# Kernel optimization log

Hardware: AMD Instinct MI355X
Metric: run time of the kernel (lower is better)

The kernel has to match this reference:

```python
import jax, jax.numpy as jnp
import numpy as np

H = 1200  # hidden size
I = 30    # input feature size


def _gru_layer(x_seq, h0, W_ih, W_hh, b_ih, b_hh):
    """x_seq: [T, B, I_in]; h0: [B, H]. PyTorch gate order (r, z, n)."""
    def step(h, x_t):
        gi = x_t @ W_ih.T + b_ih          # [B, 3H]
        gh = h @ W_hh.T + b_hh            # [B, 3H]
        i_r, i_z, i_n = jnp.split(gi, 3, axis=-1)
        h_r, h_z, h_n = jnp.split(gh, 3, axis=-1)
        r = jax.nn.sigmoid(i_r + h_r)
        z = jax.nn.sigmoid(i_z + h_z)
        n = jnp.tanh(i_n + r * h_n)
        h_new = (1.0 - z) * n + z * h
        return h_new, h_new
    h_last, outs = jax.lax.scan(step, h0, x_seq)
    return outs, h_last  # outs: [T, B, H]


def setup_inputs() -> dict:
    key = jax.random.key(0)
    ks = jax.random.split(key, 9)
    k = 1.0 / np.sqrt(H)
    u = lambda kk, shape: jax.random.uniform(kk, shape, jnp.float32, -k, k)
    x = jax.random.normal(ks[0], (64, 512, I), dtype=jnp.float32)
    return {
        "x": x,
        "W_ih0": u(ks[1], (3 * H, I)),
        "W_hh0": u(ks[2], (3 * H, H)),
        "b_ih0": u(ks[3], (3 * H,)),
        "b_hh0": u(ks[4], (3 * H,)),
        "W_ih1": u(ks[5], (3 * H, H)),
        "W_hh1": u(ks[6], (3 * H, H)),
        "b_ih1": u(ks[7], (3 * H,)),
        "b_hh1": u(ks[8], (3 * H,)),
    }


def reference(x, W_ih0, W_hh0, b_ih0, b_hh0, W_ih1, W_hh1, b_ih1, b_hh1):
    B = x.shape[0]
    x_tb = jnp.transpose(x, (1, 0, 2))  # [T, B, I]
    h0 = jnp.zeros((B, H), dtype=x.dtype)
    out0, h_last0 = _gru_layer(x_tb, h0, W_ih0, W_hh0, b_ih0, b_hh0)
    out1, h_last1 = _gru_layer(out0, h0, W_ih1, W_hh1, b_ih1, b_hh1)
    h_n = jnp.stack([h_last0, h_last1], axis=0)  # [2, B, H]
    return h_n
```

## Files before the change

kernel.cpp:

```cpp
#include <hip/hip_runtime.h>
#include <hip/hip_bf16.h>


#define Hh 1200
#define HP 1280
#define TT 512
#define II 30
#define KS_TOT 38
#define KS_PW 5
#define NTG 75
#define NBLK 225
#define NTHR 512

typedef __attribute__((ext_vector_type(8))) short short8;
typedef __attribute__((ext_vector_type(4))) float f32x4;

#define SZ_WF 17510400ull
#define OFF_WHH0 0ull
#define OFF_WIH1 SZ_WF
#define OFF_WHH1 (2ull*SZ_WF)
#define OFF_STATE (3ull*SZ_WF)
#define SZ_HF 307200ull
#define SZ_HB 163840ull
#define SZ_GX 921600ull
#define OFF_H0F OFF_STATE
#define OFF_H1F (OFF_H0F + SZ_HF)
#define OFF_H0B (OFF_H1F + SZ_HF)
#define OFF_H1B (OFF_H0B + 2ull*SZ_HB)
#define OFF_GX  (OFF_H1B + 2ull*SZ_HB)
#define STATE_BYTES (2ull*SZ_HF + 4ull*SZ_HB + 2ull*SZ_GX)
#define OFF_BAR (OFF_STATE + STATE_BYTES)
#define WS_NEEDED (OFF_BAR + 16384ull)

__device__ __forceinline__ unsigned short f2bf(float f){
  unsigned u = __float_as_uint(f);
  unsigned r = u + 0x7FFFu + ((u >> 16) & 1u);
  return (unsigned short)(r >> 16);
}
__device__ __forceinline__ float bf2f(unsigned short s){
  return __uint_as_float(((unsigned)s) << 16);
}
__device__ __forceinline__ float sigmoid_f(float v){ return 1.f/(1.f + __expf(-v)); }
__device__ __forceinline__ float tanh_f(float v){ float e = __expf(2.f*v); return 1.f - 2.f/(e + 1.f); }
__device__ __forceinline__ unsigned long long pack2f(float a, float b){
  union { float f[2]; unsigned long long u; } v; v.f[0]=a; v.f[1]=b; return v.u;
}
__device__ __forceinline__ short8 aload16(const unsigned short* p){
  union { unsigned long long u[2]; short8 s; } v;
  const unsigned long long* q = (const unsigned long long*)p;
  v.u[0] = __hip_atomic_load(q,     __ATOMIC_RELAXED, __HIP_MEMORY_SCOPE_AGENT);
  v.u[1] = __hip_atomic_load(q + 1, __ATOMIC_RELAXED, __HIP_MEMORY_SCOPE_AGENT);
  return v.s;
}
__device__ __forceinline__ void aload2f(const float* p, float* f0, float* f1){
  union { unsigned long long u; float f[2]; } v;
  v.u = __hip_atomic_load((const unsigned long long*)p, __ATOMIC_RELAXED, __HIP_MEMORY_SCOPE_AGENT);
  *f0 = v.f[0]; *f1 = v.f[1];
}

__global__ void prep_w(const float* __restrict__ W, unsigned short* __restrict__ Wf){
  int blk = blockIdx.x;
  int nt = blk / KS_TOT, ks = blk - nt*KS_TOT;
  int l = threadIdx.x;
  int n = nt*16 + (l & 15);
  int k0 = ks*32 + (l >> 4)*8;
  alignas(16) unsigned short hi[8];
  alignas(16) unsigned short lo[8];
  #pragma unroll
  for (int j = 0; j < 8; j++){
    int k = k0 + j;
    float w = (k < Hh) ? W[(size_t)n*Hh + k] : 0.f;
    unsigned short h16 = f2bf(w);
    hi[j] = h16;
    lo[j] = f2bf(w - bf2f(h16));
  }
  size_t cbase = ((size_t)(nt*KS_TOT + ks))*1024ull;
  *(short8*)(Wf + cbase + (size_t)l*8)        = *(const short8*)hi;
  *(short8*)(Wf + cbase + 512 + (size_t)l*8)  = *(const short8*)lo;
}

__global__ void init_state(char* __restrict__ ws){
  size_t i = (size_t)blockIdx.x*256 + threadIdx.x;
  size_t n_all = (STATE_BYTES + 16384ull)/16ull;
  if (i < n_all){
    f32x4 z = {0.f,0.f,0.f,0.f};
    ((f32x4*)(ws + OFF_STATE))[i] = z;
  }
}

__global__ void __launch_bounds__(NTHR)
__attribute__((amdgpu_waves_per_eu(2)))
gru_persist(
    char* __restrict__ ws,
    const float* __restrict__ x,
    const float* __restrict__ Wih0,
    const float* __restrict__ bih0, const float* __restrict__ bhh0,
    const float* __restrict__ bih1, const float* __restrict__ bhh1)
{
  const int bid  = blockIdx.x;
  const int role = bid / NTG;
  const int nb   = bid - role*NTG;
  const int tid  = threadIdx.x;
  const int wv   = tid >> 6;
  const int lane = tid & 63;
  const int col  = lane & 15;
  const int kg   = lane >> 4;
  const int ks0  = wv * KS_PW;
  const int eb  = tid >> 3;
  const int ecp = tid & 7;
  const int c0  = ecp*2;
  const int gc0 = nb*16 + c0;
  const int lastS = (role == 0) ? (TT-1) : (TT+1);

  __shared__ float part[12][8][256];
  __shared__ float red[12][256];
  __shared__ float xl[64][II];
  __shared__ float wl[48][II];
  __shared__ float hfl[64][16];

  int* bar_flags = (int*)(ws + OFF_BAR);

  for (int i = tid; i < 64*16; i += NTHR) ((float*)hfl)[i] = 0.f;

  const short8* wt = (const short8*)(ws + ((role==0)?OFF_WHH0:(role==1)?OFF_WIH1:OFF_WHH1));
  short8 wfr[3][KS_PW][2];
  #pragma unroll
  for (int g = 0; g < 3; g++)
    #pragma unroll
    for (int k = 0; k < KS_PW; k++){
      int ks = ks0 + k;
      #pragma unroll
      for (int sp = 0; sp < 2; sp++){
        short8 v = {0,0,0,0,0,0,0,0};
        if (ks < KS_TOT)
          v = wt[((size_t)((g*NTG + nb)*KS_TOT + ks))*128 + sp*64 + lane];
        wfr[g][k][sp] = v;
        asm("" : "+v"(wfr[g][k][sp]));
      }
    }

  if (role == 0){
    for (int i = tid; i < 48*II; i += NTHR){
      int rl = i/II, c = i - rl*II;
      int g = rl >> 4, cl = rl & 15;
      wl[rl][c] = Wih0[(size_t)(g*Hh + nb*16 + cl)*II + c];
    }
  }

  float bIv[3][2] = {{0.f,0.f},{0.f,0.f},{0.f,0.f}};
  float bHv[3][2] = {{0.f,0.f},{0.f,0.f},{0.f,0.f}};
  if (role == 0){
    #pragma unroll
    for (int g = 0; g < 3; g++){
      bIv[g][0] = bih0[g*Hh + gc0]; bIv[g][1] = bih0[g*Hh + gc0 + 1];
      bHv[g][0] = bhh0[g*Hh + gc0]; bHv[g][1] = bhh0[g*Hh + gc0 + 1];
    }
  } else if (role == 1){
    #pragma unroll
    for (int g = 0; g < 3; g++){
      bIv[g][0] = bih1[g*Hh + gc0]; bIv[g][1] = bih1[g*Hh + gc0 + 1];
    }
  } else {
    #pragma unroll
    for (int g = 0; g < 3; g++){
      bHv[g][0] = bhh1[g*Hh + gc0]; bHv[g][1] = bhh1[g*Hh + gc0 + 1];
    }
  }

  for (int s = 0; s < TT + 2; s++){
    const bool active = (role==0) ? (s < TT) : (role==1) ? (s >= 1 && s <= TT) : (s >= 2);
    const int t   = s - role;
    const int par = t & 1;

    if (active){
      const unsigned short* Ab;
      if (role == 0)      Ab = (const unsigned short*)(ws + OFF_H0B + (size_t)par*SZ_HB);
      else if (role == 1) Ab = (const unsigned short*)(ws + OFF_H0B + (size_t)((t+1)&1)*SZ_HB);
      else                Ab = (const unsigned short*)(ws + OFF_H1B + (size_t)par*SZ_HB);

      if (role == 0){
        for (int i = tid; i < 64*II; i += NTHR){
          int b = i/II, c = i - b*II;
          xl[b][c] = x[(size_t)b*(TT*II) + t*II + c];
        }
      }

      f32x4 acc[3][4];
      #pragma unroll
      for (int g = 0; g < 3; g++)
        #pragma unroll
        for (int m = 0; m < 4; m++) acc[g][m] = (f32x4){0.f,0.f,0.f,0.f};

      #pragma unroll
      for (int k = 0; k < KS_PW; k++){
        short8 a[4];
        #pragma unroll
        for (int m = 0; m < 4; m++)
          a[m] = aload16(&Ab[(size_t)(m*16 + col)*HP + (ks0 + k)*32 + kg*8]);
        #pragma unroll
        for (int g = 0; g < 3; g++)
          #pragma unroll
          for (int m = 0; m < 4; m++){
            acc[g][m] = __builtin_amdgcn_mfma_f32_16x16x32_bf16(a[m], wfr[g][k][0], acc[g][m], 0,0,0);
            acc[g][m] = __builtin_amdgcn_mfma_f32_16x16x32_bf16(a[m], wfr[g][k][1], acc[g][m], 0,0,0);
          }
      }
      #pragma unroll
      for (int g = 0; g < 3; g++)
        #pragma unroll
        for (int m = 0; m < 4; m++)
          *(f32x4*)&part[g*4 + m][wv][lane*4] = acc[g][m];
    }
    __syncthreads();

    if (active){
      #pragma unroll
      for (int r = 0; r < 6; r++){
        int o = r*NTHR + tid;
        int tile = o >> 8, e = o & 255;
        float v = part[tile][0][e] + part[tile][1][e] + part[tile][2][e] + part[tile][3][e]
                + part[tile][4][e] + part[tile][5][e] + part[tile][6][e] + part[tile][7][e];
        red[tile][e] = v;
      }
    }
    __syncthreads();

    if (active){
      const int mt = eb >> 4, dr = eb & 15;
      const int e0 = ((dr>>2)<<6) | (c0<<2) | (dr&3);
      if (role == 1){
        float* gxo = (float*)(ws + OFF_GX + (size_t)par*SZ_GX);
        #pragma unroll
        for (int g = 0; g < 3; g++){
          float v0 = red[g*4+mt][e0]     + bIv[g][0];
          float v1 = red[g*4+mt][e0 + 4] + bIv[g][1];
          __hip_atomic_store((unsigned long long*)&gxo[(size_t)eb*3600 + g*Hh + gc0],
                             pack2f(v0, v1), __ATOMIC_RELAXED, __HIP_MEMORY_SCOPE_AGENT);
        }
      } else {
        float gxv[3][2];
        if (role == 0){
          #pragma unroll
          for (int g = 0; g < 3; g++)
            #pragma unroll
            for (int j = 0; j < 2; j++){
              float sum = bIv[g][j];
              #pragma unroll
              for (int i = 0; i < II; i++) sum += wl[g*16 + c0 + j][i] * xl[eb][i];
              gxv[g][j] = sum;
            }
        } else {
          const float* gxi = (const float*)(ws + OFF_GX + (size_t)par*SZ_GX);
          #pragma unroll
          for (int g = 0; g < 3; g++)
            aload2f(&gxi[(size_t)eb*3600 + g*Hh + gc0], &gxv[g][0], &gxv[g][1]);
        }
        unsigned short* hbout = (unsigned short*)(ws + ((role==0)?OFF_H0B:OFF_H1B)
                                                   + (size_t)(par^1)*SZ_HB);
        float hq[2];
        unsigned short hb[2];
        #pragma unroll
        for (int j = 0; j < 2; j++){
          int e = e0 + j*4;
          float rr = sigmoid_f(red[mt][e]     + gxv[0][j] + bHv[0][j]);
          float zz = sigmoid_f(red[4+mt][e]   + gxv[1][j] + bHv[1][j]);
          float nn = tanh_f(gxv[2][j] + rr*(red[8+mt][e] + bHv[2][j]));
          float hold = hfl[eb][c0 + j];
          float hn = (1.f - zz)*nn + zz*hold;
          hfl[eb][c0 + j] = hn;
          hq[j] = hn;
          hb[j] = f2bf(hn);
        }
        unsigned pk = (unsigned)hb[0] | ((unsigned)hb[1] << 16);
        __hip_atomic_store((unsigned*)&hbout[(size_t)eb*HP + gc0], pk,
                           __ATOMIC_RELAXED, __HIP_MEMORY_SCOPE_AGENT);
        if (s == lastS){
          float* hfin = (float*)(ws + ((role==0)?OFF_H0F:OFF_H1F));
          hfin[(size_t)eb*Hh + gc0]     = hq[0];
          hfin[(size_t)eb*Hh + gc0 + 1] = hq[1];
        }
      }
    }

    __syncthreads();
    if (tid == 0){
      asm volatile("s_waitcnt vmcnt(0)" ::: "memory");
      __hip_atomic_store(&bar_flags[bid*16], s+1, __ATOMIC_RELAXED, __HIP_MEMORY_SCOPE_AGENT);
    }
    if (tid < NBLK){
      while (__hip_atomic_load(&bar_flags[tid*16], __ATOMIC_RELAXED, __HIP_MEMORY_SCOPE_AGENT) < s+1)
        __builtin_amdgcn_s_sleep(1);
    }
    asm volatile("" ::: "memory");
    __syncthreads();
  }
}

__global__ void write_out(const char* __restrict__ ws, float* __restrict__ out){
  int i = blockIdx.x*256 + threadIdx.x;
  if (i < 76800)        out[i] = *(const float*)(ws + OFF_H0F + (size_t)i*4);
  else if (i < 153600)  out[i] = *(const float*)(ws + OFF_H1F + (size_t)(i - 76800)*4);
}

extern "C" void kernel_launch(void* const* d_in, const int* in_sizes, int n_in,
                              void* d_out, int out_size, void* d_ws, size_t ws_size,
                              hipStream_t stream)
{
  const float* x    = (const float*)d_in[0];
  const float* Wih0 = (const float*)d_in[1];
  const float* Whh0 = (const float*)d_in[2];
  const float* bih0 = (const float*)d_in[3];
  const float* bhh0 = (const float*)d_in[4];
  const float* Wih1 = (const float*)d_in[5];
  const float* Whh1 = (const float*)d_in[6];
  const float* bih1 = (const float*)d_in[7];
  const float* bhh1 = (const float*)d_in[8];
  char* ws = (char*)d_ws;
  if (ws_size < WS_NEEDED) return;

  dim3 pgrid(NBLK*KS_TOT);
  prep_w<<<pgrid, 64, 0, stream>>>(Whh0, (unsigned short*)(ws + OFF_WHH0));
  prep_w<<<pgrid, 64, 0, stream>>>(Wih1, (unsigned short*)(ws + OFF_WIH1));
  prep_w<<<pgrid, 64, 0, stream>>>(Whh1, (unsigned short*)(ws + OFF_WHH1));
  init_state<<<764, 256, 0, stream>>>(ws);

  gru_persist<<<NBLK, NTHR, 0, stream>>>(ws, x, Wih0, bih0, bhh0, bih1, bhh1);

  write_out<<<600, 256, 0, stream>>>(ws, (float*)d_out);
}
```

Baseline: 7.442 ms.

## Replace global all-block barrier with per-role dependency flags and deeper buffers

Drops the 225-block global barrier run every step. Each role group (layer0 recurrent, layer1 input projection, layer1 recurrent) now waits only on the flags of the producers it depends on, with acquire/release fences, and the hidden-state buffers go from 2 to 4 so producers can run ahead of consumers. The final hidden states are written straight to the output, so the separate write_out kernel and the fp32 state buffers are removed. This cuts barrier wait and lets the layers pipeline more loosely, but the multi-buffer flag protocol is harder to get right and can race or deadlock if any wait bound is off.

```diff
diff --git a/kernel.cpp b/kernel.cpp
--- a/kernel.cpp
+++ b/kernel.cpp
@@ -19,18 +19,13 @@
 #define OFF_WHH0 0ull
 #define OFF_WIH1 SZ_WF
 #define OFF_WHH1 (2ull*SZ_WF)
-#define OFF_STATE (3ull*SZ_WF)
-#define SZ_HF 307200ull
 #define SZ_HB 163840ull
 #define SZ_GX 921600ull
-#define OFF_H0F OFF_STATE
-#define OFF_H1F (OFF_H0F + SZ_HF)
-#define OFF_H0B (OFF_H1F + SZ_HF)
-#define OFF_H1B (OFF_H0B + 2ull*SZ_HB)
-#define OFF_GX  (OFF_H1B + 2ull*SZ_HB)
-#define STATE_BYTES (2ull*SZ_HF + 4ull*SZ_HB + 2ull*SZ_GX)
-#define OFF_BAR (OFF_STATE + STATE_BYTES)
-#define WS_NEEDED (OFF_BAR + 16384ull)
+#define OFF_H0B (3ull*SZ_WF)
+#define OFF_H1B (OFF_H0B + 4ull*SZ_HB)
+#define OFF_GX  (OFF_H1B + 4ull*SZ_HB)
+#define OFF_BAR (OFF_GX + 2ull*SZ_GX)
+#define WS_NEEDED (OFF_BAR + 4096ull)
 
 __device__ __forceinline__ unsigned short f2bf(float f){
   unsigned u = __float_as_uint(f);
@@ -57,6 +52,11 @@
   v.u = __hip_atomic_load((const unsigned long long*)p, __ATOMIC_RELAXED, __HIP_MEMORY_SCOPE_AGENT);
   *f0 = v.f[0]; *f1 = v.f[1];
 }
+
+#define POLLGE(addr, thr) \
+  while (__hip_atomic_load((addr), __ATOMIC_RELAXED, __HIP_MEMORY_SCOPE_AGENT) < (thr)) \
+    __builtin_amdgcn_s_sleep(1)
+#define ACQ() __builtin_amdgcn_fence(__ATOMIC_ACQUIRE, "agent")
 
 __global__ void prep_w(const float* __restrict__ W, unsigned short* __restrict__ Wf){
   int blk = blockIdx.x;
@@ -81,12 +81,51 @@
 
 __global__ void init_state(char* __restrict__ ws){
   size_t i = (size_t)blockIdx.x*256 + threadIdx.x;
-  size_t n_all = (STATE_BYTES + 16384ull)/16ull;
+  size_t n_all = (WS_NEEDED - OFF_H0B)/16ull;
   if (i < n_all){
     f32x4 z = {0.f,0.f,0.f,0.f};
-    ((f32x4*)(ws + OFF_STATE))[i] = z;
-  }
-}
+    ((f32x4*)(ws + OFF_H0B))[i] = z;
+  }
+}
+
+#define COMPUTE_MFMA(AbPtr)                                                      \
+  {                                                                              \
+    _Pragma("unroll")                                                            \
+    for (int g = 0; g < 3; g++)                                                  \
+      _Pragma("unroll")                                                          \
+      for (int m = 0; m < 4; m++) acc[g][m] = (f32x4){0.f,0.f,0.f,0.f};          \
+    _Pragma("unroll")                                                            \
+    for (int k = 0; k < KS_PW; k++){                                             \
+      short8 a[4];                                                               \
+      _Pragma("unroll")                                                          \
+      for (int m = 0; m < 4; m++)                                                \
+        a[m] = aload16(&(AbPtr)[(size_t)(m*16 + col)*HP + (ks0 + k)*32 + kg*8]); \
+      _Pragma("unroll")                                                          \
+      for (int g = 0; g < 3; g++)                                                \
+        _Pragma("unroll")                                                        \
+        for (int m = 0; m < 4; m++){                                             \
+          acc[g][m] = __builtin_amdgcn_mfma_f32_16x16x32_bf16(a[m], wfr[g][k][0], acc[g][m], 0,0,0); \
+          acc[g][m] = __builtin_amdgcn_mfma_f32_16x16x32_bf16(a[m], wfr[g][k][1], acc[g][m], 0,0,0); \
+        }                                                                        \
+    }                                                                            \
+    _Pragma("unroll")                                                            \
+    for (int g = 0; g < 3; g++)                                                  \
+      _Pragma("unroll")                                                          \
+      for (int m = 0; m < 4; m++)                                                \
+        *(f32x4*)&part[g*4 + m][wv][lane*4] = acc[g][m];                         \
+  }
+
+#define REDUCE6()                                                                \
+  {                                                                              \
+    _Pragma("unroll")                                                            \
+    for (int r = 0; r < 6; r++){                                                 \
+      int o = r*NTHR + tid;                                                      \
+      int tile = o >> 8, e = o & 255;                                            \
+      red[tile][e] = part[tile][0][e] + part[tile][1][e] + part[tile][2][e]      \
+                   + part[tile][3][e] + part[tile][4][e] + part[tile][5][e]      \
+                   + part[tile][6][e] + part[tile][7][e];                        \
+    }                                                                            \
+  }
 
 __global__ void __launch_bounds__(NTHR)
 __attribute__((amdgpu_waves_per_eu(2)))
@@ -95,7 +134,8 @@
     const float* __restrict__ x,
     const float* __restrict__ Wih0,
     const float* __restrict__ bih0, const float* __restrict__ bhh0,
-    const float* __restrict__ bih1, const float* __restrict__ bhh1)
+    const float* __restrict__ bih1, const float* __restrict__ bhh1,
+    float* __restrict__ out)
 {
   const int bid  = blockIdx.x;
   const int role = bid / NTG;
@@ -106,11 +146,10 @@
   const int col  = lane & 15;
   const int kg   = lane >> 4;
   const int ks0  = wv * KS_PW;
-  const int eb  = tid >> 3;
-  const int ecp = tid & 7;
-  const int c0  = ecp*2;
-  const int gc0 = nb*16 + c0;
-  const int lastS = (role == 0) ? (TT-1) : (TT+1);
+  const int eb   = tid >> 3;
+  const int ecp  = tid & 7;
+  const int c0   = ecp*2;
+  const int gc0  = nb*16 + c0;
 
   __shared__ float part[12][8][256];
   __shared__ float red[12][256];
@@ -118,7 +157,9 @@
   __shared__ float wl[48][II];
   __shared__ float hfl[64][16];
 
-  int* bar_flags = (int*)(ws + OFF_BAR);
+  int* F0 = (int*)(ws + OFF_BAR);
+  int* F1 = F0 + 300;
+  int* F2 = F0 + 600;
 
   for (int i = tid; i < 64*16; i += NTHR) ((float*)hfl)[i] = 0.f;
 
@@ -167,69 +208,77 @@
     }
   }
 
-  for (int s = 0; s < TT + 2; s++){
-    const bool active = (role==0) ? (s < TT) : (role==1) ? (s >= 1 && s <= TT) : (s >= 2);
-    const int t   = s - role;
-    const int par = t & 1;
-
-    if (active){
-      const unsigned short* Ab;
-      if (role == 0)      Ab = (const unsigned short*)(ws + OFF_H0B + (size_t)par*SZ_HB);
-      else if (role == 1) Ab = (const unsigned short*)(ws + OFF_H0B + (size_t)((t+1)&1)*SZ_HB);
-      else                Ab = (const unsigned short*)(ws + OFF_H1B + (size_t)par*SZ_HB);
-
-      if (role == 0){
-        for (int i = tid; i < 64*II; i += NTHR){
-          int b = i/II, c = i - b*II;
-          xl[b][c] = x[(size_t)b*(TT*II) + t*II + c];
-        }
-      }
-
+  const int pb = 10*wv + lane;
+  const bool pw = (lane < 10) && (pb < NTG);
+
+  if (role == 0){
+    for (int s = 0; s < TT; s++){
+      for (int i = tid; i < 64*II; i += NTHR){
+        int b = i/II, c = i - b*II;
+        xl[b][c] = x[(size_t)b*(TT*II) + s*II + c];
+      }
+      if (s > 0){ if (pw) POLLGE(&F0[pb*4], s); ACQ(); }
+      const unsigned short* Ab = (const unsigned short*)(ws + OFF_H0B + (size_t)(s&3)*SZ_HB);
       f32x4 acc[3][4];
-      #pragma unroll
-      for (int g = 0; g < 3; g++)
+      COMPUTE_MFMA(Ab);
+      __syncthreads();
+      REDUCE6();
+      if (s >= 3 && tid < 75)                POLLGE(&F0[tid*4], s-2);
+      if (s >= 4 && tid >= 128 && tid < 203) POLLGE(&F1[(tid-128)*4], s-3);
+      __syncthreads();
+      {
+        const int mt = eb >> 4, dr = eb & 15;
+        const int e0 = ((dr>>2)<<6) | (c0<<2) | (dr&3);
+        unsigned short* hbout = (unsigned short*)(ws + OFF_H0B + (size_t)((s+1)&3)*SZ_HB);
+        float hq[2]; unsigned short hb2[2];
         #pragma unroll
-        for (int m = 0; m < 4; m++) acc[g][m] = (f32x4){0.f,0.f,0.f,0.f};
-
-      #pragma unroll
-      for (int k = 0; k < KS_PW; k++){
-        short8 a[4];
-        #pragma unroll
-        for (int m = 0; m < 4; m++)
-          a[m] = aload16(&Ab[(size_t)(m*16 + col)*HP + (ks0 + k)*32 + kg*8]);
-        #pragma unroll
-        for (int g = 0; g < 3; g++)
+        for (int j = 0; j < 2; j++){
+          float g0 = bIv[0][j], g1 = bIv[1][j], g2 = bIv[2][j];
           #pragma unroll
-          for (int m = 0; m < 4; m++){
-            acc[g][m] = __builtin_amdgcn_mfma_f32_16x16x32_bf16(a[m], wfr[g][k][0], acc[g][m], 0,0,0);
-            acc[g][m] = __builtin_amdgcn_mfma_f32_16x16x32_bf16(a[m], wfr[g][k][1], acc[g][m], 0,0,0);
+          for (int i = 0; i < II; i++){
+            float xv = xl[eb][i];
+            g0 += wl[c0 + j][i]      * xv;
+            g1 += wl[16 + c0 + j][i] * xv;
+            g2 += wl[32 + c0 + j][i] * xv;
           }
-      }
-      #pragma unroll
-      for (int g = 0; g < 3; g++)
-        #pragma unroll
-        for (int m = 0; m < 4; m++)
-          *(f32x4*)&part[g*4 + m][wv][lane*4] = acc[g][m];
-    }
-    __syncthreads();
-
-    if (active){
-      #pragma unroll
-      for (int r = 0; r < 6; r++){
-        int o = r*NTHR + tid;
-        int tile = o >> 8, e = o & 255;
-        float v = part[tile][0][e] + part[tile][1][e] + part[tile][2][e] + part[tile][3][e]
-                + part[tile][4][e] + part[tile][5][e] + part[tile][6][e] + part[tile][7][e];
-        red[tile][e] = v;
-      }
-    }
-    __syncthreads();
-
-    if (active){
-      const int mt = eb >> 4, dr = eb & 15;
-      const int e0 = ((dr>>2)<<6) | (c0<<2) | (dr&3);
-      if (role == 1){
-        float* gxo = (float*)(ws + OFF_GX + (size_t)par*SZ_GX);
+          int e = e0 + j*4;
+          float rr = sigmoid_f(red[mt][e]   + g0 + bHv[0][j]);
+          float zz = sigmoid_f(red[4+mt][e] + g1 + bHv[1][j]);
+          float nn = tanh_f(g2 + rr*(red[8+mt][e] + bHv[2][j]));
+          float hold = hfl[eb][c0 + j];
+          float hn = (1.f - zz)*nn + zz*hold;
+          hfl[eb][c0 + j] = hn;
+          hq[j] = hn; hb2[j] = f2bf(hn);
+        }
+        unsigned pk = (unsigned)hb2[0] | ((unsigned)hb2[1] << 16);
+        __hip_atomic_store((unsigned*)&hbout[(size_t)eb*HP + gc0], pk,
+                           __ATOMIC_RELAXED, __HIP_MEMORY_SCOPE_AGENT);
+        if (s == TT-1){
+          out[(size_t)eb*Hh + gc0]     = hq[0];
+          out[(size_t)eb*Hh + gc0 + 1] = hq[1];
+        }
+      }
+      __syncthreads();
+      if (tid == 0){
+        __builtin_amdgcn_fence(__ATOMIC_RELEASE, "agent");
+        __hip_atomic_store(&F0[nb*4], s+1, __ATOMIC_RELAXED, __HIP_MEMORY_SCOPE_AGENT);
+      }
+    }
+  } else if (role == 1){
+    for (int t = 0; t < TT; t++){
+      if (pw) POLLGE(&F0[pb*4], t+1);
+      ACQ();
+      const unsigned short* Ab = (const unsigned short*)(ws + OFF_H0B + (size_t)((t+1)&3)*SZ_HB);
+      f32x4 acc[3][4];
+      COMPUTE_MFMA(Ab);
+      __syncthreads();
+      REDUCE6();
+      if (t >= 2 && tid == 0) POLLGE(&F2[nb*4], t-1);
+      __syncthreads();
+      {
+        const int mt = eb >> 4, dr = eb & 15;
+        const int e0 = ((dr>>2)<<6) | (c0<<2) | (dr&3);
+        float* gxo = (float*)(ws + OFF_GX + (size_t)(t&1)*SZ_GX);
         #pragma unroll
         for (int g = 0; g < 3; g++){
           float v0 = red[g*4+mt][e0]     + bIv[g][0];
@@ -237,69 +286,61 @@
           __hip_atomic_store((unsigned long long*)&gxo[(size_t)eb*3600 + g*Hh + gc0],
                              pack2f(v0, v1), __ATOMIC_RELAXED, __HIP_MEMORY_SCOPE_AGENT);
         }
-      } else {
+      }
+      __syncthreads();
+      if (tid == 0){
+        __builtin_amdgcn_fence(__ATOMIC_RELEASE, "agent");
+        __hip_atomic_store(&F1[nb*4], t+1, __ATOMIC_RELAXED, __HIP_MEMORY_SCOPE_AGENT);
+      }
+    }
+  } else {
+    for (int t = 0; t < TT; t++){
+      if (t > 0){ if (pw) POLLGE(&F2[pb*4], t); ACQ(); }
+      const unsigned short* Ab = (const unsigned short*)(ws + OFF_H1B + (size_t)(t&3)*SZ_HB);
+      f32x4 acc[3][4];
+      COMPUTE_MFMA(Ab);
+      __syncthreads();
+      REDUCE6();
+      if (tid == 0) POLLGE(&F1[nb*4], t+1);
+      if (t >= 3 && tid >= 64 && tid < 139) POLLGE(&F2[(tid-64)*4], t-2);
+      ACQ();
+      __syncthreads();
+      {
+        const int mt = eb >> 4, dr = eb & 15;
+        const int e0 = ((dr>>2)<<6) | (c0<<2) | (dr&3);
+        const float* gxi = (const float*)(ws + OFF_GX + (size_t)(t&1)*SZ_GX);
+        unsigned short* hbout = (unsigned short*)(ws + OFF_H1B + (size_t)((t+1)&3)*SZ_HB);
         float gxv[3][2];
-        if (role == 0){
-          #pragma unroll
-          for (int g = 0; g < 3; g++)
-            #pragma unroll
-            for (int j = 0; j < 2; j++){
-              float sum = bIv[g][j];
-              #pragma unroll
-              for (int i = 0; i < II; i++) sum += wl[g*16 + c0 + j][i] * xl[eb][i];
-              gxv[g][j] = sum;
-            }
-        } else {
-          const float* gxi = (const float*)(ws + OFF_GX + (size_t)par*SZ_GX);
-          #pragma unroll
-          for (int g = 0; g < 3; g++)
-            aload2f(&gxi[(size_t)eb*3600 + g*Hh + gc0], &gxv[g][0], &gxv[g][1]);
-        }
-        unsigned short* hbout = (unsigned short*)(ws + ((role==0)?OFF_H0B:OFF_H1B)
-                                                   + (size_t)(par^1)*SZ_HB);
-        float hq[2];
-        unsigned short hb[2];
+        #pragma unroll
+        for (int g = 0; g < 3; g++)
+          aload2f(&gxi[(size_t)eb*3600 + g*Hh + gc0], &gxv[g][0], &gxv[g][1]);
+        float hq[2]; unsigned short hb2[2];
         #pragma unroll
         for (int j = 0; j < 2; j++){
           int e = e0 + j*4;
-          float rr = sigmoid_f(red[mt][e]     + gxv[0][j] + bHv[0][j]);
-          float zz = sigmoid_f(red[4+mt][e]   + gxv[1][j] + bHv[1][j]);
+          float rr = sigmoid_f(red[mt][e]   + gxv[0][j] + bHv[0][j]);
+          float zz = sigmoid_f(red[4+mt][e] + gxv[1][j] + bHv[1][j]);
           float nn = tanh_f(gxv[2][j] + rr*(red[8+mt][e] + bHv[2][j]));
           float hold = hfl[eb][c0 + j];
           float hn = (1.f - zz)*nn + zz*hold;
           hfl[eb][c0 + j] = hn;
-          hq[j] = hn;
-          hb[j] = f2bf(hn);
-        }
-        unsigned pk = (unsigned)hb[0] | ((unsigned)hb[1] << 16);
+          hq[j] = hn; hb2[j] = f2bf(hn);
+        }
+        unsigned pk = (unsigned)hb2[0] | ((unsigned)hb2[1] << 16);
         __hip_atomic_store((unsigned*)&hbout[(size_t)eb*HP + gc0], pk,
                            __ATOMIC_RELAXED, __HIP_MEMORY_SCOPE_AGENT);
-        if (s == lastS){
-          float* hfin = (float*)(ws + ((role==0)?OFF_H0F:OFF_H1F));
-          hfin[(size_t)eb*Hh + gc0]     = hq[0];
-          hfin[(size_t)eb*Hh + gc0 + 1] = hq[1];
-        }
-      }
-    }
-
-    __syncthreads();
-    if (tid == 0){
-      asm volatile("s_waitcnt vmcnt(0)" ::: "memory");
-      __hip_atomic_store(&bar_flags[bid*16], s+1, __ATOMIC_RELAXED, __HIP_MEMORY_SCOPE_AGENT);
-    }
-    if (tid < NBLK){
-      while (__hip_atomic_load(&bar_flags[tid*16], __ATOMIC_RELAXED, __HIP_MEMORY_SCOPE_AGENT) < s+1)
-        __builtin_amdgcn_s_sleep(1);
-    }
-    asm volatile("" ::: "memory");
-    __syncthreads();
-  }
-}
-
-__global__ void write_out(const char* __restrict__ ws, float* __restrict__ out){
-  int i = blockIdx.x*256 + threadIdx.x;
-  if (i < 76800)        out[i] = *(const float*)(ws + OFF_H0F + (size_t)i*4);
-  else if (i < 153600)  out[i] = *(const float*)(ws + OFF_H1F + (size_t)(i - 76800)*4);
+        if (t == TT-1){
+          out[76800 + (size_t)eb*Hh + gc0]     = hq[0];
+          out[76800 + (size_t)eb*Hh + gc0 + 1] = hq[1];
+        }
+      }
+      __syncthreads();
+      if (tid == 0){
+        __builtin_amdgcn_fence(__ATOMIC_RELEASE, "agent");
+        __hip_atomic_store(&F2[nb*4], t+1, __ATOMIC_RELAXED, __HIP_MEMORY_SCOPE_AGENT);
+      }
+    }
+  }
 }
 
 extern "C" void kernel_launch(void* const* d_in, const int* in_sizes, int n_in,
@@ -322,9 +363,8 @@
   prep_w<<<pgrid, 64, 0, stream>>>(Whh0, (unsigned short*)(ws + OFF_WHH0));
   prep_w<<<pgrid, 64, 0, stream>>>(Wih1, (unsigned short*)(ws + OFF_WIH1));
   prep_w<<<pgrid, 64, 0, stream>>>(Whh1, (unsigned short*)(ws + OFF_WHH1));
-  init_state<<<764, 256, 0, stream>>>(ws);
-
-  gru_persist<<<NBLK, NTHR, 0, stream>>>(ws, x, Wih0, bih0, bhh0, bih1, bhh1);
-
-  write_out<<<600, 256, 0, stream>>>(ws, (float*)d_out);
-}
+  init_state<<<772, 256, 0, stream>>>(ws);
+
+  gru_persist<<<NBLK, NTHR, 0, stream>>>(ws, x, Wih0, bih0, bhh0, bih1, bhh1,
+                                         (float*)d_out);
+}
```

New measurement: 15.31 ms. +105.7%, slower.
